# Performance work log

Measured on AMD Instinct MI355X. Metric: run time of the kernel, lower is better.

## Reference

```python
import jax, jax.numpy as jnp
import numpy as np

S, D, H, DK, DV = 4096, 1024, 16, 64, 64


def setup_inputs() -> dict:
    key = jax.random.key(0)
    ks = jax.random.split(key, 6)
    x = jax.random.normal(ks[0], (S, D), dtype=jnp.float32)
    # per-head projection weights, stacked over heads; scaled for numerical sanity
    Wq = jax.random.normal(ks[1], (H, D, DK), dtype=jnp.float32) / np.sqrt(D)
    Wk = jax.random.normal(ks[2], (H, D, DK), dtype=jnp.float32) / np.sqrt(D)
    Wv = jax.random.normal(ks[3], (H, D, DV), dtype=jnp.float32) / np.sqrt(D)
    Wc = jax.random.normal(ks[4], (H * DV, D), dtype=jnp.float32) / np.sqrt(H * DV)
    bc = jnp.zeros((D,), dtype=jnp.float32)
    return {"x": x, "Wq": Wq, "Wk": Wk, "Wv": Wv, "Wc": Wc, "bc": bc}


def reference(x, Wq, Wk, Wv, Wc, bc):
    # Per-head projections (original loops over heads with separate Linears;
    # stacking over h is the same math, vectorized).
    q = jnp.einsum("sd,hdk->hsk", x, Wq)   # [H,S,DK]
    k = jnp.einsum("sd,hdk->hsk", x, Wk)   # [H,S,DK]
    v = jnp.einsum("sd,hdv->hsv", x, Wv)   # [H,S,DV]
    scores = jnp.einsum("hsk,htk->hst", q, k) / jnp.sqrt(jnp.asarray(DK, x.dtype))
    probs = jax.nn.softmax(scores, axis=-1)  # softmax over last dim, per row
    o = jnp.einsum("hst,htv->hsv", probs, v)  # [H,S,DV]
    cat = jnp.transpose(o, (1, 0, 2)).reshape(S, H * DV)  # concat heads on last dim
    return cat @ Wc + bc  # output projection with bias
```

## Files before the change

### kernel.cpp

```cpp
#include <hip/hip_runtime.h>
#include <hip/hip_bf16.h>

#define S_ 4096
#define D_ 1024
#define H_ 16
#define DK_ 64
#define DV_ 64

typedef short bf16x8 __attribute__((ext_vector_type(8)));
typedef short bf16x4 __attribute__((ext_vector_type(4)));
typedef float floatx4 __attribute__((ext_vector_type(4)));
using bf16 = __hip_bfloat16;

#define MFMA16(a, b, c) __builtin_amdgcn_mfma_f32_16x16x32_bf16(a, b, c, 0, 0, 0)

#if __has_builtin(__builtin_amdgcn_exp2f)
#define EXP2(x) __builtin_amdgcn_exp2f(x)
#else
#define EXP2(x) exp2f(x)
#endif

__device__ __forceinline__ void stage16(const void* g, void* l) {
    __builtin_amdgcn_global_load_lds(
        (const __attribute__((address_space(1))) void*)g,
        (__attribute__((address_space(3))) void*)l, 16, 0, 0);
}

__device__ __forceinline__ bf16x8 ldsfrag(const bf16* base, int row, int chunk) {
    return *(const bf16x8*)(base + row * 64 + (((chunk ^ (row & 7))) << 3));
}
__device__ __forceinline__ bf16x8 ldsfrag32(const bf16* base, int row, int chunk) {
    return *(const bf16x8*)(base + row * 32 + (((chunk ^ (row & 3))) << 3));
}

__device__ __forceinline__ unsigned short bfbits(float f) {
    union { bf16 h; unsigned short u; } c; c.h = __float2bfloat16(f); return c.u;
}
__device__ __forceinline__ float bf2f(bf16 h) { return __bfloat162float(h); }
__device__ __forceinline__ unsigned int pkrne(float lo, float hi) {
    return (unsigned int)bfbits(lo) | ((unsigned int)bfbits(hi) << 16);
}

__device__ __forceinline__ unsigned int pktrunc(float lo, float hi) {
    union { float f; unsigned int u; } a, b;
    a.f = hi; b.f = lo;
    return __builtin_amdgcn_perm(a.u, b.u, 0x07060302u);
}

__global__ __launch_bounds__(256)
void prep(const float* __restrict__ x, const float* __restrict__ Wq,
          const float* __restrict__ Wk, const float* __restrict__ Wv,
          const float* __restrict__ Wc,
          bf16* __restrict__ xb, bf16* __restrict__ Wt, bf16* __restrict__ Wct)
{
    __shared__ float ls[64][65];
    const int bx = blockIdx.x, t = threadIdx.x;

    if (bx < 2048) {
        int i = bx * 2048 + t * 8;
        float4 a = *(const float4*)(x + i);
        float4 b = *(const float4*)(x + i + 4);
        ushort4 lo, hi;
        lo.x = bfbits(a.x); lo.y = bfbits(a.y); lo.z = bfbits(a.z); lo.w = bfbits(a.w);
        hi.x = bfbits(b.x); hi.y = bfbits(b.y); hi.z = bfbits(b.z); hi.w = bfbits(b.w);
        *(ushort4*)(xb + i) = lo;
        *(ushort4*)(xb + i + 4) = hi;
        return;
    }
    if (bx < 2816) {
        const int idx = bx - 2048;
        const int z = idx >> 4, which = z >> 4, h = z & 15;
        const float* s = (which == 0 ? Wq : which == 1 ? Wk : Wv) + (size_t)h * D_ * 64;
        bf16* d = Wt + ((size_t)which * 1024 + h * 64) * D_;
        const float scale = (which == 0) ? 0.125f * 1.44269504088896340736f : 1.0f;
        const int r0 = (idx & 15) * 64;
        {
            int r = t >> 2, cseg = (t & 3) * 16;
            const float* sp = s + (size_t)(r0 + r) * 64 + cseg;
            #pragma unroll
            for (int i = 0; i < 16; i += 4) {
                float4 v = *(const float4*)(sp + i);
                ls[r][cseg + i + 0] = v.x; ls[r][cseg + i + 1] = v.y;
                ls[r][cseg + i + 2] = v.z; ls[r][cseg + i + 3] = v.w;
            }
        }
        __syncthreads();
        {
            int c = t >> 2, rseg = (t & 3) * 16;
            bf16* dp = d + (size_t)c * D_ + r0 + rseg;
            unsigned int u[8];
            #pragma unroll
            for (int i = 0; i < 8; i++)
                u[i] = pkrne(ls[rseg + 2 * i][c] * scale, ls[rseg + 2 * i + 1][c] * scale);
            uint4 o0, o1;
            o0.x = u[0]; o0.y = u[1]; o0.z = u[2]; o0.w = u[3];
            o1.x = u[4]; o1.y = u[5]; o1.z = u[6]; o1.w = u[7];
            *(uint4*)(dp)     = o0;
            *(uint4*)(dp + 8) = o1;
        }
        return;
    }
    {
        const int idx = bx - 2816;
        const int r0 = (idx & 15) * 64, c0 = (idx >> 4) * 64;
        {
            int r = t >> 2, cseg = (t & 3) * 16;
            const float* sp = Wc + (size_t)(r0 + r) * D_ + c0 + cseg;
            #pragma unroll
            for (int i = 0; i < 16; i += 4) {
                float4 v = *(const float4*)(sp + i);
                ls[r][cseg + i + 0] = v.x; ls[r][cseg + i + 1] = v.y;
                ls[r][cseg + i + 2] = v.z; ls[r][cseg + i + 3] = v.w;
            }
        }
        __syncthreads();
        {
            int c = t >> 2, rseg = (t & 3) * 16;
            bf16* dp = Wct + (size_t)(c0 + c) * D_ + r0 + rseg;
            unsigned int u[8];
            #pragma unroll
            for (int i = 0; i < 8; i++)
                u[i] = pkrne(ls[rseg + 2 * i][c], ls[rseg + 2 * i + 1][c]);
            uint4 o0, o1;
            o0.x = u[0]; o0.y = u[1]; o0.z = u[2]; o0.w = u[3];
            o1.x = u[4]; o1.y = u[5]; o1.z = u[6]; o1.w = u[7];
            *(uint4*)(dp)     = o0;
            *(uint4*)(dp + 8) = o1;
        }
    }
}

__global__ __launch_bounds__(256)
void qkv_gemm(const bf16* __restrict__ xb, const bf16* __restrict__ Wt,
              bf16* __restrict__ Qb, bf16* __restrict__ Kb, bf16* __restrict__ Vtb)
{
    const int fid = blockIdx.x + 32 * blockIdx.y;
    const int lin = (fid & 7) * 96 + (fid >> 3);
    const int m0 = (lin & 31) * 128;
    const int n0 = (lin >> 5) * 128;
    __shared__ __align__(16) bf16 xa[2][128 * 32];
    __shared__ __align__(16) bf16 wb2[2][128 * 32];

    const int t = threadIdx.x, lane = t & 63, w = t >> 6;
    const int l15 = lane & 15, quad = lane >> 4;

    auto stage_a = [&](int buf, int kk) {
        #pragma unroll
        for (int j = 0; j < 2; j++) {
            int row = j * 64 + (t >> 2);
            int ch  = (t & 3) ^ (row & 3);
            stage16((const char*)xb + ((size_t)(m0 + row) * D_ + kk) * 2 + ch * 16,
                    (char*)&xa[buf][0] + (j * 4 + w) * 1024);
        }
    };
    auto stage_b = [&](int buf, int kk) {
        #pragma unroll
        for (int j = 0; j < 2; j++) {
            int row = j * 64 + (t >> 2);
            int ch  = (t & 3) ^ (row & 3);
            stage16((const char*)Wt + ((size_t)(n0 + row) * D_ + kk) * 2 + ch * 16,
                    (char*)&wb2[buf][0] + (j * 4 + w) * 1024);
        }
    };

    const floatx4 fz = {0.f, 0.f, 0.f, 0.f};
    floatx4 acc[2][8];
    #pragma unroll
    for (int mt = 0; mt < 2; mt++)
        #pragma unroll
        for (int nt = 0; nt < 8; nt++) acc[mt][nt] = fz;

    const int which = n0 >> 10;

    stage_a(0, 0); stage_b(0, 0);
    if (which != 2) {
        for (int kt = 0; kt < 32; kt++) {
            int cur = kt & 1;
            __syncthreads();
            if (kt < 31) { stage_a(cur ^ 1, (kt + 1) * 32); stage_b(cur ^ 1, (kt + 1) * 32); }
            bf16x8 a0 = ldsfrag32(&xa[cur][0], w * 32 + l15,      quad);
            bf16x8 a1 = ldsfrag32(&xa[cur][0], w * 32 + 16 + l15, quad);
            #pragma unroll
            for (int nt = 0; nt < 8; nt++) {
                bf16x8 b = ldsfrag32(&wb2[cur][0], nt * 16 + l15, quad);
                acc[0][nt] = MFMA16(b, a0, acc[0][nt]);
                acc[1][nt] = MFMA16(b, a1, acc[1][nt]);
            }
        }
        bf16* base = (which == 0) ? Qb : Kb;
        #pragma unroll
        for (int nt = 0; nt < 8; nt++) {
            int n  = n0 + nt * 16 + quad * 4;
            int hh = (n >> 6) & 15, col = n & 63;
            #pragma unroll
            for (int mt = 0; mt < 2; mt++) {
                int s = m0 + w * 32 + mt * 16 + l15;
                uint2 o;
                o.x = pkrne(acc[mt][nt][0], acc[mt][nt][1]);
                o.y = pkrne(acc[mt][nt][2], acc[mt][nt][3]);
                *(uint2*)(base + ((size_t)hh * S_ + s) * 64 + col) = o;
            }
        }
    } else {
        for (int kt = 0; kt < 32; kt++) {
            int cur = kt & 1;
            __syncthreads();
            if (kt < 31) { stage_a(cur ^ 1, (kt + 1) * 32); stage_b(cur ^ 1, (kt + 1) * 32); }
            bf16x8 a0 = ldsfrag32(&xa[cur][0], w * 32 + l15,      quad);
            bf16x8 a1 = ldsfrag32(&xa[cur][0], w * 32 + 16 + l15, quad);
            #pragma unroll
            for (int nt = 0; nt < 8; nt++) {
                bf16x8 b = ldsfrag32(&wb2[cur][0], nt * 16 + l15, quad);
                acc[0][nt] = MFMA16(a0, b, acc[0][nt]);
                acc[1][nt] = MFMA16(a1, b, acc[1][nt]);
            }
        }
        #pragma unroll
        for (int nt = 0; nt < 8; nt++) {
            int n = n0 + nt * 16 + l15;
            int hh = (n >> 6) & 15, col = n & 63;
            #pragma unroll
            for (int mt = 0; mt < 2; mt++) {
                int s = m0 + w * 32 + mt * 16 + quad * 4;
                uint2 o;
                o.x = pkrne(acc[mt][nt][0], acc[mt][nt][1]);
                o.y = pkrne(acc[mt][nt][2], acc[mt][nt][3]);
                *(uint2*)(Vtb + ((size_t)hh * 64 + col) * S_ + s) = o;
            }
        }
    }
}

template<int NKT, bool FULL>
__global__ __attribute__((amdgpu_waves_per_eu(2))) __launch_bounds__(256)
void attn(const bf16* __restrict__ Qb, const bf16* __restrict__ Kb,
          const bf16* __restrict__ Vtb, bf16* __restrict__ Cat,
          bf16* __restrict__ Opart, float* __restrict__ lpart)
{
    const int fid = blockIdx.x + 16 * (blockIdx.y + 16 * blockIdx.z);
    const int xcd = fid & 7, r = fid >> 3;
    const int hz  = (r >> 4) * 8 + xcd;
    const int m0   = (r & 15) * 256;
    const int h    = hz & 15;
    const int half = hz >> 4;
    const int keybase = half * (NKT * 64);

    __shared__ __align__(16) bf16 ka[2][64 * 64];
    __shared__ __align__(16) bf16 vt[2][64 * 64];

    const int t = threadIdx.x, lane = t & 63, w = t >> 6;
    const int l15 = lane & 15, quad = lane >> 4;

    auto stage_kv = [&](int buf, int key0) {
        const char* kg = (const char*)(Kb + ((size_t)h * S_ + key0) * 64);
        #pragma unroll
        for (int j = 0; j < 2; j++) {
            int c = (j * 4 + w) * 64 + lane;
            int row = c >> 3, ch = (c & 7) ^ (row & 7);
            stage16(kg + row * 128 + ch * 16, (char*)&ka[buf][0] + (j * 4 + w) * 1024);
        }
        const char* vg = (const char*)(Vtb + (size_t)h * 64 * S_ + key0);
        #pragma unroll
        for (int j = 0; j < 2; j++) {
            int c = (j * 4 + w) * 64 + lane;
            int row = c >> 3, ch = (c & 7) ^ (row & 7);
            stage16(vg + (size_t)row * (S_ * 2) + ch * 16, (char*)&vt[buf][0] + (j * 4 + w) * 1024);
        }
    };

    bf16x8 qf[4][2];
    #pragma unroll
    for (int nq = 0; nq < 4; nq++)
        #pragma unroll
        for (int ks = 0; ks < 2; ks++)
            qf[nq][ks] = *(const bf16x8*)(Qb +
                ((size_t)h * S_ + m0 + w * 64 + nq * 16 + l15) * 64 + ks * 32 + quad * 8);

    bf16x8 ones8;
    #pragma unroll
    for (int i = 0; i < 8; i++) ones8[i] = (short)0x3F80;

    const floatx4 fz = {0.f, 0.f, 0.f, 0.f};
    floatx4 acc[4][4];
    floatx4 rsa[4];
    #pragma unroll
    for (int nq = 0; nq < 4; nq++) {
        rsa[nq] = fz;
        #pragma unroll
        for (int nt = 0; nt < 4; nt++) acc[nq][nt] = fz;
    }

    stage_kv(0, keybase);
    __syncthreads();

    #pragma unroll 1
    for (int kt = 0; kt < NKT; kt++) {
        const int cur = kt & 1;
        if (kt + 1 < NKT) stage_kv(cur ^ 1, keybase + (kt + 1) * 64);

        union bf4u { bf16x4 v; unsigned int u[2]; };
        bf4u pf[4][4];
        #pragma unroll
        for (int mk = 0; mk < 4; mk++) {
            bf16x8 a0 = ldsfrag(&ka[cur][0], mk * 16 + l15, quad);
            bf16x8 a1 = ldsfrag(&ka[cur][0], mk * 16 + l15, 4 + quad);
            floatx4 s[4];
            #pragma unroll
            for (int nq = 0; nq < 4; nq++) s[nq] = fz;
            __builtin_amdgcn_s_setprio(1);
            #pragma unroll
            for (int nq = 0; nq < 4; nq++) s[nq] = MFMA16(a0, qf[nq][0], s[nq]);
            #pragma unroll
            for (int nq = 0; nq < 4; nq++) s[nq] = MFMA16(a1, qf[nq][1], s[nq]);
            __builtin_amdgcn_s_setprio(0);
            #pragma unroll
            for (int nq = 0; nq < 4; nq++) {
                float p0 = EXP2(s[nq][0]);
                float p1 = EXP2(s[nq][1]);
                float p2 = EXP2(s[nq][2]);
                float p3 = EXP2(s[nq][3]);
                pf[mk][nq].u[0] = pktrunc(p0, p1);
                pf[mk][nq].u[1] = pktrunc(p2, p3);
            }
        }

        #pragma unroll
        for (int p = 0; p < 2; p++) {
            union { bf16x8 v8; bf16x4 v4[2]; } b8[4];
            #pragma unroll
            for (int nq = 0; nq < 4; nq++) {
                b8[nq].v4[0] = pf[2 * p + 0][nq].v;
                b8[nq].v4[1] = pf[2 * p + 1][nq].v;
            }
            __builtin_amdgcn_s_setprio(1);
            #pragma unroll
            for (int nq = 0; nq < 4; nq++)
                rsa[nq] = MFMA16(ones8, b8[nq].v8, rsa[nq]);
            __builtin_amdgcn_s_setprio(0);
            #pragma unroll
            for (int nt = 0; nt < 4; nt++) {
                const char* vb = (const char*)&vt[cur][0]
                               + (nt * 16 + l15) * 128 + (quad & 1) * 8;
                const int r7 = l15 & 7;
                union { bf16x8 v8; bf16x4 v4[2]; } a8;
                a8.v4[0] = *(const bf16x4*)(vb + (((4 * p +     (quad >> 1)) ^ r7) << 4));
                a8.v4[1] = *(const bf16x4*)(vb + (((4 * p + 2 + (quad >> 1)) ^ r7) << 4));
                __builtin_amdgcn_s_setprio(1);
                #pragma unroll
                for (int nq = 0; nq < 4; nq++)
                    acc[nq][nt] = MFMA16(a8.v8, b8[nq].v8, acc[nq][nt]);
                __builtin_amdgcn_s_setprio(0);
            }
        }
        __syncthreads();
    }

    if (FULL) {
        #pragma unroll
        for (int nq = 0; nq < 4; nq++) {
            float inv = 1.0f / rsa[nq][0];
            int q = m0 + w * 64 + nq * 16 + l15;
            #pragma unroll
            for (int nt = 0; nt < 4; nt++) {
                uint2 o;
                o.x = pktrunc(acc[nq][nt][0] * inv, acc[nq][nt][1] * inv);
                o.y = pktrunc(acc[nq][nt][2] * inv, acc[nq][nt][3] * inv);
                *(uint2*)(Cat + (size_t)q * (H_ * DV_) + h * 64 + nt * 16 + quad * 4) = o;
            }
        }
    } else {
        const size_t plane = (size_t)(half * H_ + h) * S_;
        #pragma unroll
        for (int nq = 0; nq < 4; nq++) {
            int q = m0 + w * 64 + nq * 16 + l15;
            #pragma unroll
            for (int nt = 0; nt < 4; nt++) {
                uint2 o;
                o.x = pktrunc(acc[nq][nt][0], acc[nq][nt][1]);
                o.y = pktrunc(acc[nq][nt][2], acc[nq][nt][3]);
                *(uint2*)(Opart + (plane + q) * 64 + nt * 16 + quad * 4) = o;
            }
            if (quad == 0) lpart[plane + q] = rsa[nq][0];
        }
    }
}

template<int NS>
__global__ __launch_bounds__(256)
void combineN(const bf16* __restrict__ Opart, const float* __restrict__ lpart,
              bf16* __restrict__ Cat)
{
    const int h = blockIdx.y;
    const int off = (blockIdx.x * 256 + threadIdx.x) * 8;
    const int s = off >> 6, dv = off & 63;
    float a[8] = {0.f, 0.f, 0.f, 0.f, 0.f, 0.f, 0.f, 0.f};
    float l = 0.f;
    #pragma unroll
    for (int p = 0; p < NS; p++) {
        union { bf16x8 v; bf16 e[8]; } o;
        o.v = *(const bf16x8*)(Opart + (size_t)(p * H_ + h) * S_ * 64 + off);
        #pragma unroll
        for (int i = 0; i < 8; i++) a[i] += bf2f(o.e[i]);
        l += lpart[(size_t)(p * H_ + h) * S_ + s];
    }
    float inv = 1.0f / l;
    uint4 o;
    o.x = pktrunc(a[0] * inv, a[1] * inv);
    o.y = pktrunc(a[2] * inv, a[3] * inv);
    o.z = pktrunc(a[4] * inv, a[5] * inv);
    o.w = pktrunc(a[6] * inv, a[7] * inv);
    *(uint4*)(Cat + (size_t)s * (H_ * DV_) + h * 64 + dv) = o;
}

__global__ __launch_bounds__(256)
void out_proj(const bf16* __restrict__ Cat, const bf16* __restrict__ Wct,
              const float* __restrict__ bc, float* __restrict__ out)
{
    const int fid = blockIdx.x + 32 * blockIdx.y;
    const int lin = (fid & 7) * 64 + (fid >> 3);
    const int m0 = (lin & 31) * 128;
    const int n0 = (lin >> 5) * 64;
    __shared__ __align__(16) bf16 ca[2][128 * 64];
    __shared__ __align__(16) bf16 wb2[2][64 * 64];

    const int t = threadIdx.x, lane = t & 63, w = t >> 6;
    const int l15 = lane & 15, quad = lane >> 4;

    auto stage_a = [&](int buf, int kk) {
        #pragma unroll
        for (int j = 0; j < 4; j++) {
            int idx = j * 256 + t;
            int r = idx >> 3, c = idx & 7;
            int ch = c ^ (r & 7);
            stage16((const char*)Cat + ((size_t)(m0 + r) * D_ + kk + ch * 8) * 2,
                    (char*)&ca[buf][0] + (j * 4 + w) * 1024);
        }
    };
    auto stage_b = [&](int buf, int kk) {
        #pragma unroll
        for (int j = 0; j < 2; j++) {
            int idx = j * 256 + t;
            int r = idx >> 3, c = idx & 7;
            int ch = c ^ (r & 7);
            stage16((const char*)Wct + ((size_t)(n0 + r) * D_ + kk + ch * 8) * 2,
                    (char*)&wb2[buf][0] + (j * 4 + w) * 1024);
        }
    };

    const floatx4 fz = {0.f, 0.f, 0.f, 0.f};
    floatx4 acc[2][4];
    #pragma unroll
    for (int mt = 0; mt < 2; mt++)
        #pragma unroll
        for (int nt = 0; nt < 4; nt++) acc[mt][nt] = fz;

    stage_a(0, 0); stage_b(0, 0);
    for (int kt = 0; kt < 16; kt++) {
        int cur = kt & 1;
        __syncthreads();
        if (kt < 15) { stage_a(cur ^ 1, (kt + 1) * 64); stage_b(cur ^ 1, (kt + 1) * 64); }
        #pragma unroll
        for (int ks = 0; ks < 2; ks++) {
            bf16x8 a0 = ldsfrag(&ca[cur][0], w * 32 + l15,      ks * 4 + quad);
            bf16x8 a1 = ldsfrag(&ca[cur][0], w * 32 + 16 + l15, ks * 4 + quad);
            #pragma unroll
            for (int nt = 0; nt < 4; nt++) {
                bf16x8 b = ldsfrag(&wb2[cur][0], nt * 16 + l15, ks * 4 + quad);
                acc[0][nt] = MFMA16(a0, b, acc[0][nt]);
                acc[1][nt] = MFMA16(a1, b, acc[1][nt]);
            }
        }
    }

    #pragma unroll
    for (int nt = 0; nt < 4; nt++) {
        int col = n0 + nt * 16 + l15;
        float bias = bc[col];
        #pragma unroll
        for (int mt = 0; mt < 2; mt++)
            #pragma unroll
            for (int r = 0; r < 4; r++) {
                int row = m0 + w * 32 + mt * 16 + quad * 4 + r;
                out[(size_t)row * D_ + col] = acc[mt][nt][r] + bias;
            }
    }
}

extern "C" void kernel_launch(void* const* d_in, const int* in_sizes, int n_in,
                              void* d_out, int out_size, void* d_ws, size_t ws_size,
                              hipStream_t stream)
{
    const float* x  = (const float*)d_in[0];
    const float* Wq = (const float*)d_in[1];
    const float* Wk = (const float*)d_in[2];
    const float* Wv = (const float*)d_in[3];
    const float* Wc = (const float*)d_in[4];
    const float* bc = (const float*)d_in[5];
    float* out = (float*)d_out;

    bf16* xb  = (bf16*)d_ws;
    bf16* Cat = xb;
    bf16* Wt  = xb  + (size_t)S_ * D_;
    bf16* Wct = Wt  + (size_t)3 * H_ * 64 * D_;
    bf16* Qb  = Wct + (size_t)D_ * H_ * DV_;
    bf16* Kb  = Qb  + (size_t)H_ * S_ * 64;
    bf16* Vtb = Kb  + (size_t)H_ * S_ * 64;
    bf16* Opart = Vtb + (size_t)H_ * 64 * S_;

    float* lpart4 = (float*)(Opart + (size_t)4 * H_ * S_ * 64);
    float* lpart2 = (float*)(Opart + (size_t)2 * H_ * S_ * 64);
    const size_t need4 = (size_t)((char*)(lpart4 + (size_t)4 * H_ * S_) - (char*)d_ws);
    const size_t need2 = (size_t)((char*)(lpart2 + (size_t)2 * H_ * S_) - (char*)d_ws);

    prep<<<dim3(3072), 256, 0, stream>>>(x, Wq, Wk, Wv, Wc, xb, Wt, Wct);
    qkv_gemm<<<dim3(S_ / 128, 3072 / 128), 256, 0, stream>>>(xb, Wt, Qb, Kb, Vtb);

    if (ws_size >= need4) {
        attn<16, false><<<dim3(16, 16, 4), 256, 0, stream>>>(
            Qb, Kb, Vtb, Cat, Opart, lpart4);
        combineN<4><<<dim3(S_ * 64 / 2048, H_), 256, 0, stream>>>(Opart, lpart4, Cat);
    } else if (ws_size >= need2) {
        attn<32, false><<<dim3(16, 16, 2), 256, 0, stream>>>(
            Qb, Kb, Vtb, Cat, Opart, lpart2);
        combineN<2><<<dim3(S_ * 64 / 2048, H_), 256, 0, stream>>>(Opart, lpart2, Cat);
    } else {
        attn<64, true><<<dim3(16, 16, 1), 256, 0, stream>>>(
            Qb, Kb, Vtb, Cat, Opart, lpart2);
    }

    out_proj<<<dim3(S_ / 128, D_ / 64), 256, 0, stream>>>(Cat, Wct, bc, out);
}
```

Before: 223.9 us.

## Triple-buffer LDS staging in QKV and output GEMMs with vmcnt-based barriers

Both GEMM kernels (qkv_gemm and out_proj) move from double-buffered LDS with a __syncthreads at the top of each k-step to a three-buffer ring that prefetches two k-steps ahead. Each step now ends with an explicit s_waitcnt vmcnt(N) plus a barrier, which waits only for the older batch of async global-to-LDS loads and leaves the newest batch in flight. The aim is to hide more global-load latency behind the MFMA work. In exchange, LDS use per block grows by half, which may lower occupancy, and correctness now depends on the hand-counted vmcnt values.

```diff
diff --git a/kernel.cpp b/kernel.cpp
--- a/kernel.cpp
+++ b/kernel.cpp
@@ -46,6 +46,13 @@
     a.f = hi; b.f = lo;
     return __builtin_amdgcn_perm(a.u, b.u, 0x07060302u);
 }
+
+#define WAITCNT_BAR(N)                                        \
+    do {                                                      \
+        asm volatile("s_waitcnt vmcnt(" #N ")" ::: "memory"); \
+        __builtin_amdgcn_sched_barrier(0);                    \
+        __builtin_amdgcn_s_barrier();                         \
+    } while (0)
 
 __global__ __launch_bounds__(256)
 void prep(const float* __restrict__ x, const float* __restrict__ Wq,
@@ -138,13 +145,13 @@
     const int lin = (fid & 7) * 96 + (fid >> 3);
     const int m0 = (lin & 31) * 128;
     const int n0 = (lin >> 5) * 128;
-    __shared__ __align__(16) bf16 xa[2][128 * 32];
-    __shared__ __align__(16) bf16 wb2[2][128 * 32];
+    __shared__ __align__(16) bf16 xa[3][128 * 32];
+    __shared__ __align__(16) bf16 wb2[3][128 * 32];
 
     const int t = threadIdx.x, lane = t & 63, w = t >> 6;
     const int l15 = lane & 15, quad = lane >> 4;
 
-    auto stage_a = [&](int buf, int kk) {
+    auto stage_ab = [&](int buf, int kk) {
         #pragma unroll
         for (int j = 0; j < 2; j++) {
             int row = j * 64 + (t >> 2);
@@ -152,8 +159,6 @@
             stage16((const char*)xb + ((size_t)(m0 + row) * D_ + kk) * 2 + ch * 16,
                     (char*)&xa[buf][0] + (j * 4 + w) * 1024);
         }
-    };
-    auto stage_b = [&](int buf, int kk) {
         #pragma unroll
         for (int j = 0; j < 2; j++) {
             int row = j * 64 + (t >> 2);
@@ -172,12 +177,15 @@
 
     const int which = n0 >> 10;
 
-    stage_a(0, 0); stage_b(0, 0);
+    stage_ab(0, 0);
+    stage_ab(1, 32);
+    WAITCNT_BAR(4);
+
     if (which != 2) {
+        #pragma unroll 1
         for (int kt = 0; kt < 32; kt++) {
-            int cur = kt & 1;
-            __syncthreads();
-            if (kt < 31) { stage_a(cur ^ 1, (kt + 1) * 32); stage_b(cur ^ 1, (kt + 1) * 32); }
+            const int cur = kt % 3;
+            if (kt + 2 < 32) stage_ab((kt + 2) % 3, (kt + 2) * 32);
             bf16x8 a0 = ldsfrag32(&xa[cur][0], w * 32 + l15,      quad);
             bf16x8 a1 = ldsfrag32(&xa[cur][0], w * 32 + 16 + l15, quad);
             #pragma unroll
@@ -185,6 +193,9 @@
                 bf16x8 b = ldsfrag32(&wb2[cur][0], nt * 16 + l15, quad);
                 acc[0][nt] = MFMA16(b, a0, acc[0][nt]);
                 acc[1][nt] = MFMA16(b, a1, acc[1][nt]);
+            }
+            if (kt + 1 < 32) {
+                if (kt + 2 < 32) { WAITCNT_BAR(4); } else { WAITCNT_BAR(0); }
             }
         }
         bf16* base = (which == 0) ? Qb : Kb;
@@ -202,10 +213,10 @@
             }
         }
     } else {
+        #pragma unroll 1
         for (int kt = 0; kt < 32; kt++) {
-            int cur = kt & 1;
-            __syncthreads();
-            if (kt < 31) { stage_a(cur ^ 1, (kt + 1) * 32); stage_b(cur ^ 1, (kt + 1) * 32); }
+            const int cur = kt % 3;
+            if (kt + 2 < 32) stage_ab((kt + 2) % 3, (kt + 2) * 32);
             bf16x8 a0 = ldsfrag32(&xa[cur][0], w * 32 + l15,      quad);
             bf16x8 a1 = ldsfrag32(&xa[cur][0], w * 32 + 16 + l15, quad);
             #pragma unroll
@@ -213,6 +224,9 @@
                 bf16x8 b = ldsfrag32(&wb2[cur][0], nt * 16 + l15, quad);
                 acc[0][nt] = MFMA16(a0, b, acc[0][nt]);
                 acc[1][nt] = MFMA16(a1, b, acc[1][nt]);
+            }
+            if (kt + 1 < 32) {
+                if (kt + 2 < 32) { WAITCNT_BAR(4); } else { WAITCNT_BAR(0); }
             }
         }
         #pragma unroll
@@ -420,13 +434,13 @@
     const int lin = (fid & 7) * 64 + (fid >> 3);
     const int m0 = (lin & 31) * 128;
     const int n0 = (lin >> 5) * 64;
-    __shared__ __align__(16) bf16 ca[2][128 * 64];
-    __shared__ __align__(16) bf16 wb2[2][64 * 64];
+    __shared__ __align__(16) bf16 ca[3][128 * 64];
+    __shared__ __align__(16) bf16 wb2[3][64 * 64];
 
     const int t = threadIdx.x, lane = t & 63, w = t >> 6;
     const int l15 = lane & 15, quad = lane >> 4;
 
-    auto stage_a = [&](int buf, int kk) {
+    auto stage_ab = [&](int buf, int kk) {
         #pragma unroll
         for (int j = 0; j < 4; j++) {
             int idx = j * 256 + t;
@@ -435,8 +449,6 @@
             stage16((const char*)Cat + ((size_t)(m0 + r) * D_ + kk + ch * 8) * 2,
                     (char*)&ca[buf][0] + (j * 4 + w) * 1024);
         }
-    };
-    auto stage_b = [&](int buf, int kk) {
         #pragma unroll
         for (int j = 0; j < 2; j++) {
             int idx = j * 256 + t;
@@ -454,11 +466,14 @@
         #pragma unroll
         for (int nt = 0; nt < 4; nt++) acc[mt][nt] = fz;
 
-    stage_a(0, 0); stage_b(0, 0);
+    stage_ab(0, 0);
+    stage_ab(1, 64);
+    WAITCNT_BAR(6);
+
+    #pragma unroll 1
     for (int kt = 0; kt < 16; kt++) {
-        int cur = kt & 1;
-        __syncthreads();
-        if (kt < 15) { stage_a(cur ^ 1, (kt + 1) * 64); stage_b(cur ^ 1, (kt + 1) * 64); }
+        const int cur = kt % 3;
+        if (kt + 2 < 16) stage_ab((kt + 2) % 3, (kt + 2) * 64);
         #pragma unroll
         for (int ks = 0; ks < 2; ks++) {
             bf16x8 a0 = ldsfrag(&ca[cur][0], w * 32 + l15,      ks * 4 + quad);
@@ -469,6 +484,9 @@
                 acc[0][nt] = MFMA16(a0, b, acc[0][nt]);
                 acc[1][nt] = MFMA16(a1, b, acc[1][nt]);
             }
+        }
+        if (kt + 1 < 16) {
+            if (kt + 2 < 16) { WAITCNT_BAR(6); } else { WAITCNT_BAR(0); }
         }
     }
 
```

Result: faster. 219.3 us, median of 3 (-2.0%).
